# Kernel tuning notes

Measured on AMD Instinct MI355X. Metric: run time of the kernel, lower is better.

Reference implementation:

```python
import jax, jax.numpy as jnp
import numpy as np

T, B, D, H, R = 256, 64, 1024, 1024, 256
S = 0.1  # winit uniform bound


def setup_inputs() -> dict:
    key = jax.random.key(0)
    ks = jax.random.split(key, 11)
    u = lambda k, shape: jax.random.uniform(k, shape, jnp.float32, -S, S)
    return {
        "x": jax.random.normal(ks[0], (T, B, D), jnp.float32),
        "h0": jnp.zeros((B, H), jnp.float32),
        "c0": jnp.zeros((B, H), jnp.float32),
        "u_x": u(ks[1], (D, R)),
        "u_h": u(ks[2], (H, R)),
        "w_x": u(ks[3], (4 * H, R)),
        "w_h": u(ks[4], (4 * H, R)),
        "b_x": u(ks[5], (4 * H,)),
        "b_h": u(ks[6], (4 * H,)),
        "dia_x": u(ks[7], (1, D)),
        "dia_h": u(ks[8], (1, H)),
    }


def reference(x, h0, c0, u_x, u_h, w_x, w_h, b_x, b_h, dia_x, dia_h):
    hidden = h0.shape[1]
    # Per-gate diagonal correction: coef[g, d] = sum_r u[d, r] * w[g*H + d, r]
    coef_x = jnp.einsum('dr,gdr->gd', u_x, w_x.reshape(4, hidden, -1)).reshape(-1)  # [4H]
    coef_h = jnp.einsum('dr,gdr->gd', u_h, w_h.reshape(4, hidden, -1)).reshape(-1)  # [4H]

    def step(carry, x_t):
        h, c = carry
        vm_x = jnp.tile(dia_x * x_t, (1, 4))            # [B,4H]
        vm_h = jnp.tile(dia_h * h, (1, 4))              # [B,4H]
        low_x = (x_t @ u_x) @ w_x.T                     # [B,4H] low-rank input proj
        low_h = (h @ u_h) @ w_h.T                       # [B,4H] low-rank hidden proj
        ref_x = jnp.tile(x_t, (1, 4)) * coef_x          # vm_refined_x
        ref_h = jnp.tile(h, (1, 4)) * coef_h            # vm_refined_h
        gx = vm_x + low_x - ref_x + b_x
        gh = vm_h + low_h - ref_h + b_h
        xi, xf, xo, xn = jnp.split(gx, 4, axis=1)
        hi, hf, ho, hn = jnp.split(gh, 4, axis=1)
        i = jax.nn.sigmoid(xi + hi)
        f = jax.nn.sigmoid(xf + hf)
        o = jax.nn.sigmoid(xo + ho)
        n = jnp.tanh(xn + hn)
        c_new = f * c + i * n
        h_new = o * jnp.tanh(c_new)
        return (h_new, c_new), h_new

    (h_f, c_f), outputs = jax.lax.scan(step, (h0, c0), x)
    return outputs, h_f, c_f
```

## Files before the change

kernel.cpp:

```cpp
#include <hip/hip_runtime.h>
#include <stdint.h>

#define T_STEPS 256
#define BATCH 64
#define DIM 1024
#define HID 1024
#define RANK 256
#define FOURH 4096
#define M1 (T_STEPS * BATCH)

typedef __bf16 bf16_t;
typedef bf16_t bf16x8 __attribute__((ext_vector_type(8)));
typedef float f32x4 __attribute__((ext_vector_type(4)));

union frag_cast { uint4 u; bf16x8 v; };
union b_cast { unsigned long long ll[2]; bf16x8 v; };

__device__ __forceinline__ bf16x8 load_frag(const unsigned short* p) {
  frag_cast c; c.u = *reinterpret_cast<const uint4*>(p); return c.v;
}
__device__ __forceinline__ unsigned short f2bf(float f) {
  union { float f; uint32_t u; } v; v.f = f;
  uint32_t u = v.u;
  return (unsigned short)((u + 0x7fffu + ((u >> 16) & 1u)) >> 16);
}
__device__ __forceinline__ float bf2f(unsigned short h) {
  union { uint32_t u; float f; } v; v.u = ((uint32_t)h) << 16; return v.f;
}
__device__ __forceinline__ float fsig(float x) {
  return __builtin_amdgcn_rcpf(1.f + __expf(-x));
}
__device__ __forceinline__ float ftanh(float x) {
  return 1.f - 2.f * __builtin_amdgcn_rcpf(1.f + __expf(2.f * x));
}

__global__ void k_pack(const float* __restrict__ src, unsigned short* __restrict__ dst,
                       int NT, int ld, int transposed) {
  int id = blockIdx.x * blockDim.x + threadIdx.x;
  int lane = id & 63;
  int fi = id >> 6;
  int nt = fi % NT, kc = fi / NT;
  int k0 = kc * 32 + ((lane >> 4) * 8);
  int n  = nt * 16 + (lane & 15);
  unsigned short vals[8];
  if (transposed) {
    const float* p = src + (size_t)n * ld + k0;
#pragma unroll
    for (int s = 0; s < 8; ++s) vals[s] = f2bf(p[s]);
  } else {
#pragma unroll
    for (int s = 0; s < 8; ++s) vals[s] = f2bf(src[(size_t)(k0 + s) * ld + n]);
  }
  union { unsigned short u16[8]; uint4 u; } o;
#pragma unroll
  for (int s = 0; s < 8; ++s) o.u16[s] = vals[s];
  *reinterpret_cast<uint4*>(dst + (size_t)id * 8) = o.u;
}

__global__ void k_coef(const float* __restrict__ u_x, const float* __restrict__ w_x,
                       const float* __restrict__ dia_x,
                       const float* __restrict__ b_x, const float* __restrict__ b_h,
                       float* __restrict__ corr, float* __restrict__ bias) {
  int wv = threadIdx.x >> 6, lane = threadIdx.x & 63;
  int j = blockIdx.x * 4 + wv;
  int e = j & (HID - 1);
  const float* up = u_x + (size_t)e * RANK + lane * 4;
  const float* wp = w_x + (size_t)j * RANK + lane * 4;
  float s = up[0] * wp[0] + up[1] * wp[1] + up[2] * wp[2] + up[3] * wp[3];
#pragma unroll
  for (int off = 32; off > 0; off >>= 1) s += __shfl_xor(s, off, 64);
  if (lane == 0) {
    corr[j] = dia_x[e] - s;
    bias[j] = b_x[j] + b_h[j];
  }
}

__global__ void k_init(const float* __restrict__ h0, uint32_t* __restrict__ hbuf) {
  int i = blockIdx.x * blockDim.x + threadIdx.x;
  hbuf[i] = (uint32_t)f2bf(h0[i]);
  hbuf[BATCH * HID + i] = 0xFFFF0000u;
}

__global__ void k_gemm_a32(const float* __restrict__ A, int lda,
                           const unsigned short* __restrict__ packB, int NTtot,
                           int KC, unsigned short* __restrict__ C, int ldc,
                           const float* __restrict__ dia) {
  int w = threadIdx.x >> 6, lane = threadIdx.x & 63;
  int q = lane >> 4, ln = lane & 15;
  int m0 = blockIdx.y * 64, n0 = blockIdx.x * 64;
  int arow = m0 + w * 16 + ln;
  f32x4 acc[4] = {};
  for (int kc = 0; kc < KC; ++kc) {
    const float* ap = A + (size_t)arow * lda + kc * 32 + q * 8;
    float4 x0 = *reinterpret_cast<const float4*>(ap);
    float4 x1 = *reinterpret_cast<const float4*>(ap + 4);
    bf16x8 a;
    a[0] = (bf16_t)x0.x; a[1] = (bf16_t)x0.y; a[2] = (bf16_t)x0.z; a[3] = (bf16_t)x0.w;
    a[4] = (bf16_t)x1.x; a[5] = (bf16_t)x1.y; a[6] = (bf16_t)x1.z; a[7] = (bf16_t)x1.w;
#pragma unroll
    for (int nt = 0; nt < 4; ++nt) {
      bf16x8 b = load_frag(packB + ((size_t)(kc * NTtot + blockIdx.x * 4 + nt) * 64 + lane) * 8);
      acc[nt] = __builtin_amdgcn_mfma_f32_16x16x32_bf16(a, b, acc[nt], 0, 0, 0);
    }
  }
#pragma unroll
  for (int nt = 0; nt < 4; ++nt) {
    int ccol = n0 + nt * 16 + ln;
#pragma unroll
    for (int r = 0; r < 4; ++r) {
      int crow = m0 + w * 16 + q * 4 + r;
      float v = acc[nt][r];
      if (dia != nullptr && ccol == (crow & (HID - 1))) v = dia[ccol];
      C[(size_t)crow * ldc + ccol] = f2bf(v);
    }
  }
}

__global__ void k_packAh(const unsigned short* __restrict__ AhT, unsigned short* __restrict__ dst) {
  int id = blockIdx.x * blockDim.x + threadIdx.x;
  int lane = id & 63;
  int fi = id >> 6;
  int kc = fi & 31;
  int g  = (fi >> 5) & 3;
  int cg = fi >> 7;
  int j  = g * HID + cg * 16 + (lane & 15);
  int d0 = kc * 32 + ((lane >> 4) * 8);
  uint4 v = *reinterpret_cast<const uint4*>(AhT + (size_t)j * HID + d0);
  *reinterpret_cast<uint4*>(dst + (size_t)id * 8) = v;
}

__global__ void k_gemm2(const unsigned short* __restrict__ P,
                        const unsigned short* __restrict__ packWx,
                        const float* __restrict__ x,
                        const float* __restrict__ corr, const float* __restrict__ bias,
                        unsigned short* __restrict__ gx) {
  int w = threadIdx.x >> 6, lane = threadIdx.x & 63;
  int q = lane >> 4, ln = lane & 15;
  int m0 = blockIdx.y * 64, n0 = blockIdx.x * 64;
  int arow = m0 + w * 16 + ln;
  f32x4 acc[4] = {};
#pragma unroll
  for (int kc = 0; kc < 8; ++kc) {
    bf16x8 a = load_frag(P + (size_t)arow * RANK + kc * 32 + q * 8);
#pragma unroll
    for (int nt = 0; nt < 4; ++nt) {
      bf16x8 b = load_frag(packWx + ((size_t)(kc * 256 + blockIdx.x * 4 + nt) * 64 + lane) * 8);
      acc[nt] = __builtin_amdgcn_mfma_f32_16x16x32_bf16(a, b, acc[nt], 0, 0, 0);
    }
  }
#pragma unroll
  for (int nt = 0; nt < 4; ++nt) {
    int j = n0 + nt * 16 + ln;
    int e = j & (HID - 1);
    float cj = corr[j], bj = bias[j];
#pragma unroll
    for (int r = 0; r < 4; ++r) {
      int m = m0 + w * 16 + q * 4 + r;
      float v = acc[nt][r] + x[(size_t)m * DIM + e] * cj + bj;
      gx[(size_t)m * FOURH + j] = f2bf(v);
    }
  }
}

__global__ __launch_bounds__(256, 1) __attribute__((amdgpu_waves_per_eu(1, 1)))
void k_rec(
    const unsigned short* __restrict__ pAh,
    const unsigned short* __restrict__ gx,
    const float* __restrict__ c0,
    uint32_t* __restrict__ hbuf,
    float* __restrict__ out) {
  const int tid = threadIdx.x;
  const int g = tid >> 6, lane = tid & 63;
  const int q = lane >> 4, ln = lane & 15;
  const int blk = blockIdx.x;
  const int cg2 = blk & 31, bg = blk >> 5;

  unsigned long long bqa0[32], bqb0[32], bqa1[32], bqb1[32];
  {
    const unsigned long long* p0 = reinterpret_cast<const unsigned long long*>(pAh) +
        (((size_t)((2 * cg2 + 0) * 4 + g) * 32) * 64 + lane) * 2;
    const unsigned long long* p1 = reinterpret_cast<const unsigned long long*>(pAh) +
        (((size_t)((2 * cg2 + 1) * 4 + g) * 32) * 64 + lane) * 2;
#pragma unroll
    for (int kc = 0; kc < 32; ++kc) {
      bqa0[kc] = *reinterpret_cast<const volatile unsigned long long*>(p0 + (size_t)kc * 128);
      bqb0[kc] = *reinterpret_cast<const volatile unsigned long long*>(p0 + (size_t)kc * 128 + 1);
      bqa1[kc] = *reinterpret_cast<const volatile unsigned long long*>(p1 + (size_t)kc * 128);
      bqb1[kc] = *reinterpret_cast<const volatile unsigned long long*>(p1 + (size_t)kc * 128 + 1);
    }
  }

  const int rb = tid >> 4, ec = tid & 15;
  const int brow = bg * 16 + rb;
  const int e0 = cg2 * 32 + 2 * ec;
  float c_a = c0[brow * HID + e0];
  float c_b = c0[brow * HID + e0 + 1];

  __shared__ unsigned short hstage[16][1032];
  __shared__ float pre[4][16][34];

  size_t g0 = (size_t)brow * FOURH;
  uint32_t gxv0 = *reinterpret_cast<const uint32_t*>(gx + g0 + e0);
  uint32_t gxv1 = *reinterpret_cast<const uint32_t*>(gx + g0 + HID + e0);
  uint32_t gxv2 = *reinterpret_cast<const uint32_t*>(gx + g0 + 2 * HID + e0);
  uint32_t gxv3 = *reinterpret_cast<const uint32_t*>(gx + g0 + 3 * HID + e0);

  for (int t = 0; t < T_STEPS; ++t) {
    const int cur = t & 1;
    const uint32_t* hb = hbuf + (size_t)cur * (BATCH * HID);
    const unsigned tagexp = (unsigned)t;

    uint4 rr[16];
    unsigned pend = 0xFFFFu;
    do {
#pragma unroll
      for (int i = 0; i < 16; ++i)
        if (pend & (1u << i)) {
          const uint32_t* p = hb + (((size_t)(bg * 16 + i)) << 10) + (tid << 2);
          asm volatile("global_load_dwordx4 %0, %1, off sc1"
                       : "=&v"(rr[i]) : "v"(p) : "memory");
        }
      asm volatile("s_waitcnt vmcnt(0)" ::: "memory");
      __builtin_amdgcn_sched_barrier(0);
#pragma unroll
      for (int i = 0; i < 16; ++i)
        if (pend & (1u << i)) {
          unsigned bad = ((rr[i].x >> 16) ^ tagexp) | ((rr[i].y >> 16) ^ tagexp) |
                         ((rr[i].z >> 16) ^ tagexp) | ((rr[i].w >> 16) ^ tagexp);
          if (bad == 0) {
            unsigned lo = (rr[i].x & 0xffffu) | (rr[i].y << 16);
            unsigned hi = (rr[i].z & 0xffffu) | (rr[i].w << 16);
            *reinterpret_cast<unsigned long long*>(&hstage[i][tid << 2]) =
                ((unsigned long long)hi << 32) | lo;
            pend &= ~(1u << i);
          }
        }
    } while (pend);
    __syncthreads();

    const int tn = (t + 1 < T_STEPS) ? (t + 1) : t;
    const size_t gn = ((size_t)tn * BATCH + brow) * FOURH;
    uint32_t ngx0 = *reinterpret_cast<const uint32_t*>(gx + gn + e0);
    uint32_t ngx1 = *reinterpret_cast<const uint32_t*>(gx + gn + HID + e0);
    uint32_t ngx2 = *reinterpret_cast<const uint32_t*>(gx + gn + 2 * HID + e0);
    uint32_t ngx3 = *reinterpret_cast<const uint32_t*>(gx + gn + 3 * HID + e0);

    f32x4 acc00 = {}, acc01 = {}, acc10 = {}, acc11 = {};
#pragma unroll
    for (int kc = 0; kc < 32; kc += 2) {
      bf16x8 aA = load_frag(&hstage[ln][kc * 32 + q * 8]);
      bf16x8 aB = load_frag(&hstage[ln][(kc + 1) * 32 + q * 8]);
      b_cast b00, b01, b10, b11;
      b00.ll[0] = bqa0[kc];     b00.ll[1] = bqb0[kc];
      b01.ll[0] = bqa1[kc];     b01.ll[1] = bqb1[kc];
      b10.ll[0] = bqa0[kc + 1]; b10.ll[1] = bqb0[kc + 1];
      b11.ll[0] = bqa1[kc + 1]; b11.ll[1] = bqb1[kc + 1];
      acc00 = __builtin_amdgcn_mfma_f32_16x16x32_bf16(aA, b00.v, acc00, 0, 0, 0);
      acc01 = __builtin_amdgcn_mfma_f32_16x16x32_bf16(aA, b01.v, acc01, 0, 0, 0);
      acc10 = __builtin_amdgcn_mfma_f32_16x16x32_bf16(aB, b10.v, acc10, 0, 0, 0);
      acc11 = __builtin_amdgcn_mfma_f32_16x16x32_bf16(aB, b11.v, acc11, 0, 0, 0);
    }
#pragma unroll
    for (int r = 0; r < 4; ++r) {
      pre[g][q * 4 + r][ln]      = acc00[r] + acc10[r];
      pre[g][q * 4 + r][16 + ln] = acc01[r] + acc11[r];
    }
    __syncthreads();

    float2 p0 = *reinterpret_cast<const float2*>(&pre[0][rb][2 * ec]);
    float2 p1 = *reinterpret_cast<const float2*>(&pre[1][rb][2 * ec]);
    float2 p2 = *reinterpret_cast<const float2*>(&pre[2][rb][2 * ec]);
    float2 p3 = *reinterpret_cast<const float2*>(&pre[3][rb][2 * ec]);

    float ia = fsig(p0.x + bf2f((unsigned short)(gxv0 & 0xffffu)));
    float fa = fsig(p1.x + bf2f((unsigned short)(gxv1 & 0xffffu)));
    float oa = fsig(p2.x + bf2f((unsigned short)(gxv2 & 0xffffu)));
    float na = ftanh(p3.x + bf2f((unsigned short)(gxv3 & 0xffffu)));
    c_a = fa * c_a + ia * na;
    float hn_a = oa * ftanh(c_a);
    float ib = fsig(p0.y + bf2f((unsigned short)(gxv0 >> 16)));
    float fb = fsig(p1.y + bf2f((unsigned short)(gxv1 >> 16)));
    float ob = fsig(p2.y + bf2f((unsigned short)(gxv2 >> 16)));
    float nb = ftanh(p3.y + bf2f((unsigned short)(gxv3 >> 16)));
    c_b = fb * c_b + ib * nb;
    float hn_b = ob * ftanh(c_b);

    {
      unsigned tg = ((unsigned)(t + 1)) << 16;
      unsigned long long wv =
          (unsigned long long)(tg | (unsigned)f2bf(hn_a)) |
          ((unsigned long long)(tg | (unsigned)f2bf(hn_b)) << 32);
      __hip_atomic_store(
          reinterpret_cast<unsigned long long*>(
              hbuf + (size_t)(cur ^ 1) * (BATCH * HID) + ((size_t)brow << 10) + e0),
          wv, __ATOMIC_RELAXED, __HIP_MEMORY_SCOPE_AGENT);
    }

    {
      float2 hv; hv.x = hn_a; hv.y = hn_b;
      *reinterpret_cast<float2*>(&out[((size_t)t * BATCH + brow) * HID + e0]) = hv;
      if (t == T_STEPS - 1) {
        float2 cv; cv.x = c_a; cv.y = c_b;
        *reinterpret_cast<float2*>(
            &out[(size_t)T_STEPS * BATCH * HID + brow * HID + e0]) = hv;
        *reinterpret_cast<float2*>(
            &out[(size_t)T_STEPS * BATCH * HID + BATCH * HID + brow * HID + e0]) = cv;
      }
    }

    gxv0 = ngx0; gxv1 = ngx1; gxv2 = ngx2; gxv3 = ngx3;
  }
}

extern "C" void kernel_launch(void* const* d_in, const int* in_sizes, int n_in,
                              void* d_out, int out_size, void* d_ws, size_t ws_size,
                              hipStream_t stream) {
  const float* x     = (const float*)d_in[0];
  const float* h0    = (const float*)d_in[1];
  const float* c0    = (const float*)d_in[2];
  const float* u_x   = (const float*)d_in[3];
  const float* u_h   = (const float*)d_in[4];
  const float* w_x   = (const float*)d_in[5];
  const float* w_h   = (const float*)d_in[6];
  const float* b_x   = (const float*)d_in[7];
  const float* b_h   = (const float*)d_in[8];
  const float* dia_x = (const float*)d_in[9];
  const float* dia_h = (const float*)d_in[10];
  float* out = (float*)d_out;
  (void)in_sizes; (void)n_in; (void)out_size; (void)ws_size;

  char* base = (char*)d_ws;
  size_t off = 0;
  auto alloc = [&](size_t bytes) -> void* {
    void* p = base + off;
    off = (off + bytes + 255) & ~(size_t)255;
    return p;
  };
  unsigned short* pUx  = (unsigned short*)alloc((size_t)32 * 16 * 64 * 8 * 2);
  unsigned short* pUhT = (unsigned short*)alloc((size_t)8 * 64 * 64 * 8 * 2);
  unsigned short* pWx  = (unsigned short*)alloc((size_t)8 * 256 * 64 * 8 * 2);
  float* corr = (float*)alloc((size_t)FOURH * 4);
  float* bias = (float*)alloc((size_t)FOURH * 4);
  uint32_t* hbufT = (uint32_t*)alloc((size_t)2 * BATCH * HID * 4);
  unsigned short* P    = (unsigned short*)alloc((size_t)M1 * RANK * 2);
  unsigned short* AhT  = (unsigned short*)alloc((size_t)FOURH * HID * 2);
  unsigned short* pAh  = (unsigned short*)alloc((size_t)64 * 4 * 32 * 64 * 8 * 2);
  unsigned short* gx   = (unsigned short*)alloc((size_t)M1 * FOURH * 2);

  k_pack<<<128, 256, 0, stream>>>(u_x, pUx, 16, RANK, 0);
  k_pack<<<128, 256, 0, stream>>>(u_h, pUhT, 64, RANK, 1);
  k_pack<<<512, 256, 0, stream>>>(w_x, pWx, 256, RANK, 1);
  k_coef<<<1024, 256, 0, stream>>>(u_x, w_x, dia_x, b_x, b_h, corr, bias);
  k_init<<<256, 256, 0, stream>>>(h0, hbufT);
  k_gemm_a32<<<dim3(4, 256), 256, 0, stream>>>(x, DIM, pUx, 16, 32, P, RANK, nullptr);
  k_gemm_a32<<<dim3(16, 64), 256, 0, stream>>>(w_h, RANK, pUhT, 64, 8, AhT, HID, dia_h);
  k_packAh<<<2048, 256, 0, stream>>>(AhT, pAh);
  k_gemm2<<<dim3(64, 256), 256, 0, stream>>>(P, pWx, x, corr, bias, gx);
  k_rec<<<128, 256, 0, stream>>>(pAh, gx, c0, hbufT, out);
}
```

Baseline: 1.622 ms.

## Split recurrent matmul across 8 waves per block with register-resident weights

Doubles the recurrent kernel's block size to 512 threads so each wave owns one 16-column gate tile instead of two. That halves the per-wave MFMA chain and the register-held weight fragments. The h polling loads are spread over 512 threads (8 per thread instead of 16), and weights move into named scalars through macros so they stay in registers. Only the first 256 threads do the gate nonlinearity and the stores, so the extra waves add barrier cost and sit idle during the elementwise phase.

```diff
diff --git a/kernel.cpp b/kernel.cpp
--- a/kernel.cpp
+++ b/kernel.cpp
@@ -162,7 +162,18 @@
   }
 }
 
-__global__ __launch_bounds__(256, 1) __attribute__((amdgpu_waves_per_eu(1, 1)))
+#define KC_EACH(X) \
+  X(0) X(1) X(2) X(3) X(4) X(5) X(6) X(7) \
+  X(8) X(9) X(10) X(11) X(12) X(13) X(14) X(15) \
+  X(16) X(17) X(18) X(19) X(20) X(21) X(22) X(23) \
+  X(24) X(25) X(26) X(27) X(28) X(29) X(30) X(31)
+#define KC_ACC(X) \
+  X(0,0) X(1,1) X(2,2) X(3,3) X(4,0) X(5,1) X(6,2) X(7,3) \
+  X(8,0) X(9,1) X(10,2) X(11,3) X(12,0) X(13,1) X(14,2) X(15,3) \
+  X(16,0) X(17,1) X(18,2) X(19,3) X(20,0) X(21,1) X(22,2) X(23,3) \
+  X(24,0) X(25,1) X(26,2) X(27,3) X(28,0) X(29,1) X(30,2) X(31,3)
+
+__global__ __launch_bounds__(512, 1) __attribute__((amdgpu_waves_per_eu(2, 2)))
 void k_rec(
     const unsigned short* __restrict__ pAh,
     const unsigned short* __restrict__ gx,
@@ -170,122 +181,128 @@
     uint32_t* __restrict__ hbuf,
     float* __restrict__ out) {
   const int tid = threadIdx.x;
-  const int g = tid >> 6, lane = tid & 63;
+  const int w = tid >> 6, lane = tid & 63;
   const int q = lane >> 4, ln = lane & 15;
   const int blk = blockIdx.x;
   const int cg2 = blk & 31, bg = blk >> 5;
-
-  unsigned long long bqa0[32], bqb0[32], bqa1[32], bqb1[32];
-  {
-    const unsigned long long* p0 = reinterpret_cast<const unsigned long long*>(pAh) +
-        (((size_t)((2 * cg2 + 0) * 4 + g) * 32) * 64 + lane) * 2;
-    const unsigned long long* p1 = reinterpret_cast<const unsigned long long*>(pAh) +
-        (((size_t)((2 * cg2 + 1) * 4 + g) * 32) * 64 + lane) * 2;
-#pragma unroll
-    for (int kc = 0; kc < 32; ++kc) {
-      bqa0[kc] = *reinterpret_cast<const volatile unsigned long long*>(p0 + (size_t)kc * 128);
-      bqb0[kc] = *reinterpret_cast<const volatile unsigned long long*>(p0 + (size_t)kc * 128 + 1);
-      bqa1[kc] = *reinterpret_cast<const volatile unsigned long long*>(p1 + (size_t)kc * 128);
-      bqb1[kc] = *reinterpret_cast<const volatile unsigned long long*>(p1 + (size_t)kc * 128 + 1);
-    }
-  }
-
-  const int rb = tid >> 4, ec = tid & 15;
+  const int g = w & 3, ch2 = w >> 2;
+  const int cg_eff = cg2 * 2 + ch2;
+
+  const unsigned long long* pp = reinterpret_cast<const unsigned long long*>(pAh) +
+                                 ((size_t)((cg_eff * 4 + g) * 32) * 64 + lane) * 2;
+#define DECLB(k) unsigned long long BA_##k, BB_##k;
+  KC_EACH(DECLB)
+#undef DECLB
+#define LOADB(k) \
+  BA_##k = *reinterpret_cast<const volatile unsigned long long*>(pp + (size_t)(k) * 128); \
+  BB_##k = *reinterpret_cast<const volatile unsigned long long*>(pp + (size_t)(k) * 128 + 1);
+  KC_EACH(LOADB)
+#undef LOADB
+
+  const int rb = (tid & 255) >> 4, ec = tid & 15;
   const int brow = bg * 16 + rb;
   const int e0 = cg2 * 32 + 2 * ec;
-  float c_a = c0[brow * HID + e0];
-  float c_b = c0[brow * HID + e0 + 1];
+  float c_a = 0.f, c_b = 0.f;
+  if (tid < 256) {
+    c_a = c0[brow * HID + e0];
+    c_b = c0[brow * HID + e0 + 1];
+  }
 
   __shared__ unsigned short hstage[16][1032];
   __shared__ float pre[4][16][34];
 
-  size_t g0 = (size_t)brow * FOURH;
-  uint32_t gxv0 = *reinterpret_cast<const uint32_t*>(gx + g0 + e0);
-  uint32_t gxv1 = *reinterpret_cast<const uint32_t*>(gx + g0 + HID + e0);
-  uint32_t gxv2 = *reinterpret_cast<const uint32_t*>(gx + g0 + 2 * HID + e0);
-  uint32_t gxv3 = *reinterpret_cast<const uint32_t*>(gx + g0 + 3 * HID + e0);
+  uint32_t gxv0 = 0, gxv1 = 0, gxv2 = 0, gxv3 = 0;
+  if (tid < 256) {
+    size_t g0 = (size_t)brow * FOURH;
+    gxv0 = *reinterpret_cast<const uint32_t*>(gx + g0 + e0);
+    gxv1 = *reinterpret_cast<const uint32_t*>(gx + g0 + HID + e0);
+    gxv2 = *reinterpret_cast<const uint32_t*>(gx + g0 + 2 * HID + e0);
+    gxv3 = *reinterpret_cast<const uint32_t*>(gx + g0 + 3 * HID + e0);
+  }
 
   for (int t = 0; t < T_STEPS; ++t) {
     const int cur = t & 1;
     const uint32_t* hb = hbuf + (size_t)cur * (BATCH * HID);
     const unsigned tagexp = (unsigned)t;
 
-    uint4 rr[16];
-    unsigned pend = 0xFFFFu;
+    uint4 r0, r1, r2, r3, r4, r5, r6, r7;
+    unsigned pend = 0xFFu;
     do {
-#pragma unroll
-      for (int i = 0; i < 16; ++i)
-        if (pend & (1u << i)) {
-          const uint32_t* p = hb + (((size_t)(bg * 16 + i)) << 10) + (tid << 2);
-          asm volatile("global_load_dwordx4 %0, %1, off sc1"
-                       : "=&v"(rr[i]) : "v"(p) : "memory");
-        }
+#define ISSUE16(cc, rr)                                                        \
+      if (pend & (1u << cc)) {                                                 \
+        int ch = cc * 512 + tid;                                               \
+        const uint32_t* p = hb + (((size_t)(bg * 16 + (ch >> 8))) << 10) +     \
+                            ((ch & 255) << 2);                                 \
+        asm volatile("global_load_dwordx4 %0, %1, off sc1"                     \
+                     : "=&v"(rr) : "v"(p) : "memory");                         \
+      }
+      ISSUE16(0, r0) ISSUE16(1, r1) ISSUE16(2, r2) ISSUE16(3, r3)
+      ISSUE16(4, r4) ISSUE16(5, r5) ISSUE16(6, r6) ISSUE16(7, r7)
+#undef ISSUE16
       asm volatile("s_waitcnt vmcnt(0)" ::: "memory");
       __builtin_amdgcn_sched_barrier(0);
-#pragma unroll
-      for (int i = 0; i < 16; ++i)
-        if (pend & (1u << i)) {
-          unsigned bad = ((rr[i].x >> 16) ^ tagexp) | ((rr[i].y >> 16) ^ tagexp) |
-                         ((rr[i].z >> 16) ^ tagexp) | ((rr[i].w >> 16) ^ tagexp);
-          if (bad == 0) {
-            unsigned lo = (rr[i].x & 0xffffu) | (rr[i].y << 16);
-            unsigned hi = (rr[i].z & 0xffffu) | (rr[i].w << 16);
-            *reinterpret_cast<unsigned long long*>(&hstage[i][tid << 2]) =
-                ((unsigned long long)hi << 32) | lo;
-            pend &= ~(1u << i);
-          }
-        }
+#define CHECK16(cc, rr)                                                        \
+      if (pend & (1u << cc)) {                                                 \
+        unsigned bad = ((rr.x >> 16) ^ tagexp) | ((rr.y >> 16) ^ tagexp) |     \
+                       ((rr.z >> 16) ^ tagexp) | ((rr.w >> 16) ^ tagexp);      \
+        if (bad == 0) {                                                        \
+          int ch = cc * 512 + tid;                                             \
+          unsigned lo = (rr.x & 0xffffu) | (rr.y << 16);                       \
+          unsigned hi = (rr.z & 0xffffu) | (rr.w << 16);                       \
+          *reinterpret_cast<unsigned long long*>(                              \
+              &hstage[ch >> 8][(ch & 255) << 2]) =                             \
+              ((unsigned long long)hi << 32) | lo;                             \
+          pend &= ~(1u << cc);                                                 \
+        }                                                                      \
+      }
+      CHECK16(0, r0) CHECK16(1, r1) CHECK16(2, r2) CHECK16(3, r3)
+      CHECK16(4, r4) CHECK16(5, r5) CHECK16(6, r6) CHECK16(7, r7)
+#undef CHECK16
     } while (pend);
     __syncthreads();
 
-    const int tn = (t + 1 < T_STEPS) ? (t + 1) : t;
-    const size_t gn = ((size_t)tn * BATCH + brow) * FOURH;
-    uint32_t ngx0 = *reinterpret_cast<const uint32_t*>(gx + gn + e0);
-    uint32_t ngx1 = *reinterpret_cast<const uint32_t*>(gx + gn + HID + e0);
-    uint32_t ngx2 = *reinterpret_cast<const uint32_t*>(gx + gn + 2 * HID + e0);
-    uint32_t ngx3 = *reinterpret_cast<const uint32_t*>(gx + gn + 3 * HID + e0);
-
-    f32x4 acc00 = {}, acc01 = {}, acc10 = {}, acc11 = {};
-#pragma unroll
-    for (int kc = 0; kc < 32; kc += 2) {
-      bf16x8 aA = load_frag(&hstage[ln][kc * 32 + q * 8]);
-      bf16x8 aB = load_frag(&hstage[ln][(kc + 1) * 32 + q * 8]);
-      b_cast b00, b01, b10, b11;
-      b00.ll[0] = bqa0[kc];     b00.ll[1] = bqb0[kc];
-      b01.ll[0] = bqa1[kc];     b01.ll[1] = bqb1[kc];
-      b10.ll[0] = bqa0[kc + 1]; b10.ll[1] = bqb0[kc + 1];
-      b11.ll[0] = bqa1[kc + 1]; b11.ll[1] = bqb1[kc + 1];
-      acc00 = __builtin_amdgcn_mfma_f32_16x16x32_bf16(aA, b00.v, acc00, 0, 0, 0);
-      acc01 = __builtin_amdgcn_mfma_f32_16x16x32_bf16(aA, b01.v, acc01, 0, 0, 0);
-      acc10 = __builtin_amdgcn_mfma_f32_16x16x32_bf16(aB, b10.v, acc10, 0, 0, 0);
-      acc11 = __builtin_amdgcn_mfma_f32_16x16x32_bf16(aB, b11.v, acc11, 0, 0, 0);
-    }
-#pragma unroll
-    for (int r = 0; r < 4; ++r) {
-      pre[g][q * 4 + r][ln]      = acc00[r] + acc10[r];
-      pre[g][q * 4 + r][16 + ln] = acc01[r] + acc11[r];
-    }
+    uint32_t ngx0 = 0, ngx1 = 0, ngx2 = 0, ngx3 = 0;
+    if (tid < 256) {
+      const int tn = (t + 1 < T_STEPS) ? (t + 1) : t;
+      const size_t gn = ((size_t)tn * BATCH + brow) * FOURH;
+      ngx0 = *reinterpret_cast<const uint32_t*>(gx + gn + e0);
+      ngx1 = *reinterpret_cast<const uint32_t*>(gx + gn + HID + e0);
+      ngx2 = *reinterpret_cast<const uint32_t*>(gx + gn + 2 * HID + e0);
+      ngx3 = *reinterpret_cast<const uint32_t*>(gx + gn + 3 * HID + e0);
+    }
+
+    f32x4 acc0 = {}, acc1 = {}, acc2 = {}, acc3 = {};
+#define MF(k, c) {                                                             \
+      bf16x8 a = load_frag(&hstage[ln][(k) * 32 + q * 8]);                     \
+      b_cast b; b.ll[0] = BA_##k; b.ll[1] = BB_##k;                            \
+      acc##c = __builtin_amdgcn_mfma_f32_16x16x32_bf16(a, b.v, acc##c, 0, 0, 0); \
+    }
+    KC_ACC(MF)
+#undef MF
+#pragma unroll
+    for (int r = 0; r < 4; ++r)
+      pre[g][q * 4 + r][ch2 * 16 + ln] = (acc0[r] + acc1[r]) + (acc2[r] + acc3[r]);
     __syncthreads();
 
-    float2 p0 = *reinterpret_cast<const float2*>(&pre[0][rb][2 * ec]);
-    float2 p1 = *reinterpret_cast<const float2*>(&pre[1][rb][2 * ec]);
-    float2 p2 = *reinterpret_cast<const float2*>(&pre[2][rb][2 * ec]);
-    float2 p3 = *reinterpret_cast<const float2*>(&pre[3][rb][2 * ec]);
-
-    float ia = fsig(p0.x + bf2f((unsigned short)(gxv0 & 0xffffu)));
-    float fa = fsig(p1.x + bf2f((unsigned short)(gxv1 & 0xffffu)));
-    float oa = fsig(p2.x + bf2f((unsigned short)(gxv2 & 0xffffu)));
-    float na = ftanh(p3.x + bf2f((unsigned short)(gxv3 & 0xffffu)));
-    c_a = fa * c_a + ia * na;
-    float hn_a = oa * ftanh(c_a);
-    float ib = fsig(p0.y + bf2f((unsigned short)(gxv0 >> 16)));
-    float fb = fsig(p1.y + bf2f((unsigned short)(gxv1 >> 16)));
-    float ob = fsig(p2.y + bf2f((unsigned short)(gxv2 >> 16)));
-    float nb = ftanh(p3.y + bf2f((unsigned short)(gxv3 >> 16)));
-    c_b = fb * c_b + ib * nb;
-    float hn_b = ob * ftanh(c_b);
-
-    {
+    if (tid < 256) {
+      float2 p0 = *reinterpret_cast<const float2*>(&pre[0][rb][2 * ec]);
+      float2 p1 = *reinterpret_cast<const float2*>(&pre[1][rb][2 * ec]);
+      float2 p2 = *reinterpret_cast<const float2*>(&pre[2][rb][2 * ec]);
+      float2 p3 = *reinterpret_cast<const float2*>(&pre[3][rb][2 * ec]);
+
+      float ia = fsig(p0.x + bf2f((unsigned short)(gxv0 & 0xffffu)));
+      float fa = fsig(p1.x + bf2f((unsigned short)(gxv1 & 0xffffu)));
+      float oa = fsig(p2.x + bf2f((unsigned short)(gxv2 & 0xffffu)));
+      float na = ftanh(p3.x + bf2f((unsigned short)(gxv3 & 0xffffu)));
+      c_a = fa * c_a + ia * na;
+      float hn_a = oa * ftanh(c_a);
+      float ib = fsig(p0.y + bf2f((unsigned short)(gxv0 >> 16)));
+      float fb = fsig(p1.y + bf2f((unsigned short)(gxv1 >> 16)));
+      float ob = fsig(p2.y + bf2f((unsigned short)(gxv2 >> 16)));
+      float nb = ftanh(p3.y + bf2f((unsigned short)(gxv3 >> 16)));
+      c_b = fb * c_b + ib * nb;
+      float hn_b = ob * ftanh(c_b);
+
       unsigned tg = ((unsigned)(t + 1)) << 16;
       unsigned long long wv =
           (unsigned long long)(tg | (unsigned)f2bf(hn_a)) |
@@ -294,9 +311,7 @@
           reinterpret_cast<unsigned long long*>(
               hbuf + (size_t)(cur ^ 1) * (BATCH * HID) + ((size_t)brow << 10) + e0),
           wv, __ATOMIC_RELAXED, __HIP_MEMORY_SCOPE_AGENT);
-    }
-
-    {
+
       float2 hv; hv.x = hn_a; hv.y = hn_b;
       *reinterpret_cast<float2*>(&out[((size_t)t * BATCH + brow) * HID + e0]) = hv;
       if (t == T_STEPS - 1) {
@@ -306,9 +321,8 @@
         *reinterpret_cast<float2*>(
             &out[(size_t)T_STEPS * BATCH * HID + BATCH * HID + brow * HID + e0]) = cv;
       }
-    }
-
-    gxv0 = ngx0; gxv1 = ngx1; gxv2 = ngx2; gxv3 = ngx3;
+      gxv0 = ngx0; gxv1 = ngx1; gxv2 = ngx2; gxv3 = ngx3;
+    }
   }
 }
 
@@ -356,5 +370,5 @@
   k_gemm_a32<<<dim3(16, 64), 256, 0, stream>>>(w_h, RANK, pUhT, 64, 8, AhT, HID, dia_h);
   k_packAh<<<2048, 256, 0, stream>>>(AhT, pAh);
   k_gemm2<<<dim3(64, 256), 256, 0, stream>>>(P, pWx, x, corr, bias, gx);
-  k_rec<<<128, 256, 0, stream>>>(pAh, gx, c0, hbufT, out);
-}
+  k_rec<<<128, 512, 0, stream>>>(pAh, gx, c0, hbufT, out);
+}
```

Measured after the change: 1.380 ms. -14.9%, faster.
